# Kernel optimization log

Measured on AMD Instinct MI355X. Metric: run time of the kernel, lower is better.

## Reference

```python
import jax, jax.numpy as jnp
import numpy as np

B, T, C, H, K = 4, 2048, 1024, 16, 64
CHUNK = 64
NUM_LAYERS, LAYER_ID = 12, 6
D_MIX, D_DECAY = 32, 64


def setup_inputs() -> dict:
    key = jax.random.key(0)
    ks = jax.random.split(key, 12)
    x = jax.random.normal(ks[0], (B, T, C), jnp.float32)
    shift_state_in = jax.random.normal(ks[1], (B, C), jnp.float32)
    wkv_state_in = jnp.zeros((B, H, K, K), jnp.float32)

    r01 = LAYER_ID / max(NUM_LAYERS - 1, 1)
    r10 = 1.0 - LAYER_ID / NUM_LAYERS
    ddd = (np.arange(C, dtype=np.float64) / C)
    maa = lambda p: jnp.asarray((1.0 - ddd ** p).reshape(1, 1, C), jnp.float32)
    time_maa_x = maa(r10)
    time_maa_w = maa(r10)
    time_maa_k = maa(r10)
    time_maa_v = jnp.asarray((1.0 - (ddd ** r10 + 0.3 * r01)).reshape(1, 1, C), jnp.float32)
    time_maa_r = maa(0.5 * r10)
    time_maa_g = maa(0.5 * r10)
    time_maa_w1 = jax.random.uniform(ks[2], (C, D_MIX * 5), jnp.float32, -0.01, 0.01)
    time_maa_w2 = jax.random.uniform(ks[3], (5, D_MIX, C), jnp.float32, -0.01, 0.01)

    n = np.arange(C, dtype=np.float64)
    time_decay = jnp.asarray((-6 + 5 * (n / (C - 1)) ** (0.7 + 1.3 * r01)).reshape(1, 1, C), jnp.float32)
    time_decay_w1 = jax.random.uniform(ks[4], (C, D_DECAY), jnp.float32, -0.01, 0.01)
    time_decay_w2 = jax.random.uniform(ks[5], (D_DECAY, C), jnp.float32, -0.01, 0.01)

    zig = ((n + 1) % 3 - 1) * 0.1
    time_faaaa = jnp.asarray((r01 * (1 - n / (C - 1)) + zig).reshape(H, K), jnp.float32)
    lucid_temperature = jnp.ones((1, H, 1, 1), jnp.float32)

    s = 0.02
    W_r = jax.random.normal(ks[6], (C, C), jnp.float32) * s
    W_k = jax.random.normal(ks[7], (C, C), jnp.float32) * s
    W_v = jax.random.normal(ks[8], (C, C), jnp.float32) * s
    W_g = jax.random.normal(ks[9], (C, C), jnp.float32) * s
    W_o = jax.random.normal(ks[10], (C, C), jnp.float32) * s
    ln_gamma = jnp.ones((C,), jnp.float32)
    ln_beta = jnp.zeros((C,), jnp.float32)

    return dict(x=x, shift_state_in=shift_state_in, wkv_state_in=wkv_state_in,
                time_maa_x=time_maa_x, time_maa_w=time_maa_w, time_maa_k=time_maa_k,
                time_maa_v=time_maa_v, time_maa_r=time_maa_r, time_maa_g=time_maa_g,
                time_maa_w1=time_maa_w1, time_maa_w2=time_maa_w2,
                time_decay=time_decay, time_decay_w1=time_decay_w1, time_decay_w2=time_decay_w2,
                time_faaaa=time_faaaa, lucid_temperature=lucid_temperature,
                W_r=W_r, W_k=W_k, W_v=W_v, W_g=W_g, W_o=W_o,
                ln_gamma=ln_gamma, ln_beta=ln_beta)


def _forward(x, shift_state_in, wkv_state_in, time_maa_x, time_maa_w, time_maa_k,
             time_maa_v, time_maa_r, time_maa_g, time_maa_w1, time_maa_w2,
             time_decay, time_decay_w1, time_decay_w2, time_faaaa, lucid_temperature,
             W_r, W_k, W_v, W_g, W_o, ln_gamma, ln_beta):
    # ddlerp token shift
    dxprev = jnp.concatenate([shift_state_in[:, None, :], x[:, :-1]], axis=1) - x
    xxx = jnp.tanh((x + dxprev * time_maa_x) @ time_maa_w1).reshape(B, T, 5, D_MIX)
    m = jnp.einsum('btfd,fdc->fbtc', xxx, time_maa_w2)  # (5,B,T,C)
    mw, mk, mv, mr, mg = m[0], m[1], m[2], m[3], m[4]
    xw = x + dxprev * (time_maa_w + mw)
    xk = x + dxprev * (time_maa_k + mk)
    xv = x + dxprev * (time_maa_v + mv)
    xr = x + dxprev * (time_maa_r + mr)
    xg = x + dxprev * (time_maa_g + mg)

    r = xr @ W_r.T
    k = xk @ W_k.T
    v = xv @ W_v.T
    g = jax.nn.silu(xg @ W_g.T)
    w = time_decay + jnp.tanh(xw @ time_decay_w1) @ time_decay_w2

    tohead = lambda a: a.reshape(B, T, H, K).transpose(0, 2, 1, 3)  # (B,H,T,K)
    r_h, k_h, v_h = tohead(r), tohead(k), tohead(v)
    w_h = -jnp.exp(tohead(w))  # log-decay, negative
    u = time_faaaa.reshape(1, H, 1, K)
    temp = jax.nn.softplus(lucid_temperature)  # (1,H,1,1)

    n_chunks = T // CHUNK
    tochunks = lambda a: a.reshape(B, H, n_chunks, CHUNK, K).transpose(2, 0, 1, 3, 4)
    eye = jnp.eye(CHUNK, dtype=jnp.float32)
    mid = CHUNK // 2

    def step(state, inp):
        r_c, k_c, v_c, w_log = inp  # each (B,H,cs,K)
        w_cum = jnp.cumsum(w_log, axis=-2)
        w_shift = jnp.pad(w_cum[..., :-1, :], ((0, 0), (0, 0), (1, 0), (0, 0)))
        offset = w_shift[..., mid:mid + 1, :]
        r_decay = jnp.exp(jnp.clip(w_shift - offset, -30, 30))
        k_inv_decay = jnp.exp(jnp.clip(offset - w_cum, -30, 30))
        A = jnp.einsum('bhtk,bhsk->bhts', r_c * r_decay, k_c * k_inv_decay)
        A = jnp.tril(A, -1) + eye * jnp.sum(r_c * (u * k_c), axis=-1)[..., None]
        k_norm = k_c / jnp.maximum(jnp.linalg.norm(k_c, axis=-1, keepdims=True), 1e-12)
        K_gram = jnp.einsum('bhtk,bhsk->bhts', k_norm, k_norm)
        P = eye + jnp.exp(jnp.clip(temp * K_gram, -20, 20))
        P_v = jnp.linalg.solve(P, v_c)
        w_intra = jnp.exp(jnp.clip(w_cum - w_log, -30, 30))
        y = A @ P_v + (r_c * w_intra) @ state
        w_sum = jnp.sum(w_log, axis=-2, keepdims=True)  # (B,H,1,K)
        w_inter = jnp.exp(jnp.clip(w_sum - w_cum, -30, 30))
        new_state = state * jnp.exp(w_sum) + jnp.einsum('bhtk,bhtv->bhkv', k_c * w_inter, v_c)
        return new_state, y

    state_out, ys = jax.lax.scan(
        step, wkv_state_in,
        (tochunks(r_h), tochunks(k_h), tochunks(v_h), tochunks(w_h)))
    # (n,B,H,cs,K) -> (B,T,C)
    y = ys.transpose(1, 2, 0, 3, 4).reshape(B, H, T, K).transpose(0, 2, 1, 3).reshape(B, T, C)

    # GroupNorm with n_head groups, eps = 1e-5 * head_size_divisor**2
    eps = 1e-5 * 64.0
    yg = y.reshape(B, T, H, K)
    mu = yg.mean(axis=-1, keepdims=True)
    var = yg.var(axis=-1, keepdims=True)
    yn = (yg - mu) / jnp.sqrt(var + eps)
    yn = yn * ln_gamma.reshape(1, 1, H, K) + ln_beta.reshape(1, 1, H, K)
    yn = yn.reshape(B, T, C)

    out = (yn * g) @ W_o.T
    return out, x[:, -1], state_out


def reference(x, shift_state_in, wkv_state_in, time_maa_x, time_maa_w, time_maa_k,
              time_maa_v, time_maa_r, time_maa_g, time_maa_w1, time_maa_w2,
              time_decay, time_decay_w1, time_decay_w2, time_faaaa, lucid_temperature,
              W_r, W_k, W_v, W_g, W_o, ln_gamma, ln_beta):
    return _forward(x, shift_state_in, wkv_state_in, time_maa_x, time_maa_w, time_maa_k,
                    time_maa_v, time_maa_r, time_maa_g, time_maa_w1, time_maa_w2,
                    time_decay, time_decay_w1, time_decay_w2, time_faaaa, lucid_temperature,
                    W_r, W_k, W_v, W_g, W_o, ln_gamma, ln_beta)
```

## Files before the change

kernel.cpp:

```cpp
#include <hip/hip_runtime.h>
#include <cstdint>
#include <cstddef>

typedef unsigned short ushort_t;
#define DEVI __device__ __forceinline__

constexpr int Bc = 4, Tc = 2048, Cc = 1024, Hc = 16;
constexpr int BT = Bc * Tc;
constexpr int NCHUNK = Tc / 64;

using f32x4  = __attribute__((ext_vector_type(4))) float;
using bf16x8 = __attribute__((ext_vector_type(8))) __bf16;

DEVI ushort_t f2bf(float f) {
  union { float f; unsigned u; } v; v.f = f;
  unsigned r = v.u + 0x7fffu + ((v.u >> 16) & 1u);
  return (ushort_t)(r >> 16);
}
DEVI float bf2f(ushort_t u) {
  union { unsigned u; float f; } v; v.u = ((unsigned)u) << 16; return v.f;
}
DEVI float clip30(float x) { return fminf(fmaxf(x, -30.f), 30.f); }
DEVI float clip20(float x) { return fminf(fmaxf(x, -20.f), 20.f); }

DEVI float4 bf4up(uint2 r) {
  float4 v;
  v.x = bf2f((ushort_t)(r.x & 0xffff)); v.y = bf2f((ushort_t)(r.x >> 16));
  v.z = bf2f((ushort_t)(r.y & 0xffff)); v.w = bf2f((ushort_t)(r.y >> 16));
  return v;
}
DEVI uint2 f4pk(float4 v) {
  uint2 r;
  r.x = (unsigned)f2bf(v.x) | ((unsigned)f2bf(v.y) << 16);
  r.y = (unsigned)f2bf(v.z) | ((unsigned)f2bf(v.w) << 16);
  return r;
}

DEVI void gload_lds16(const ushort_t* g, ushort_t* l) {
  __builtin_amdgcn_global_load_lds(
      (const __attribute__((address_space(1))) void*)g,
      (__attribute__((address_space(3))) void*)l, 16, 0, 0);
}

#define GETEL(V4, E) ((E) == 0 ? (V4).x : (E) == 1 ? (V4).y : (E) == 2 ? (V4).z : (V4).w)
#define SETEL(V4, E, VAL) do { if ((E) == 0) (V4).x = (VAL); else if ((E) == 1) (V4).y = (VAL); \
                               else if ((E) == 2) (V4).z = (VAL); else (V4).w = (VAL); } while (0)

__global__ void k_xlast(const float* __restrict__ x, float* __restrict__ out) {
  int i = blockIdx.x * 256 + threadIdx.x;
  if (i >= Bc * Cc) return;
  int b = i >> 10, c = i & 1023;
  out[i] = x[((size_t)b * Tc + Tc - 1) * Cc + c];
}

__global__ void k_f2bf5(const float* __restrict__ i0, const float* __restrict__ i1,
                        const float* __restrict__ i2, const float* __restrict__ i3,
                        const float* __restrict__ i4,
                        ushort_t* __restrict__ o0, ushort_t* __restrict__ o1,
                        ushort_t* __restrict__ o2, ushort_t* __restrict__ o3,
                        ushort_t* __restrict__ o4) {
  int z = blockIdx.z;
  const float* in = (z == 0) ? i0 : (z == 1) ? i1 : (z == 2) ? i2 : (z == 3) ? i3 : i4;
  ushort_t* out   = (z == 0) ? o0 : (z == 1) ? o1 : (z == 2) ? o2 : (z == 3) ? o3 : o4;
  int i = blockIdx.x * 256 + threadIdx.x;
  if (i < Cc * Cc) out[i] = f2bf(in[i]);
}

__global__ void k_w2t(const float* __restrict__ w2, ushort_t* __restrict__ w2t) {
  int i = blockIdx.x * 256 + threadIdx.x;
  if (i >= 160 * 1024) return;
  int c = i / 160, fd = i % 160;
  w2t[i] = f2bf(w2[(size_t)fd * 1024 + c]);
}

__global__ void k_transp(const float* __restrict__ in, ushort_t* __restrict__ out, int N) {
  int i = blockIdx.x * 256 + threadIdx.x;
  if (i >= N * 1024) return;
  int n = i >> 10, r = i & 1023;
  out[i] = f2bf(in[(size_t)r * N + n]);
}

__global__ __launch_bounds__(256) void k_shift_tanh(
    const float* __restrict__ x, const float* __restrict__ sst,
    const float* __restrict__ tmx, const ushort_t* __restrict__ Wt,
    ushort_t* __restrict__ outv) {
  constexpr int NCOLS = 160, NF = NCOLS / 16;
  int tid = threadIdx.x;
  int wave = tid >> 6, lane = tid & 63;
  int row0 = (blockIdx.x * 4 + wave) * 16;
  int lr = lane & 15, lk = (lane >> 4) * 8;
  int rg = row0 + lr;
  int tt = rg & (Tc - 1);
  const float* xrow = x + (size_t)rg * Cc;
  const float* prow = (tt == 0) ? (sst + (size_t)(rg >> 11) * Cc) : (xrow - Cc);
  f32x4 acc[NF];
  #pragma unroll
  for (int n = 0; n < NF; ++n) acc[n] = (f32x4){0.f, 0.f, 0.f, 0.f};
  for (int k0 = 0; k0 < 1024; k0 += 32) {
    int c0 = k0 + lk;
    float4 xa = *(const float4*)(xrow + c0), xb = *(const float4*)(xrow + c0 + 4);
    float4 pa = *(const float4*)(prow + c0), pb = *(const float4*)(prow + c0 + 4);
    float4 ta = *(const float4*)(tmx + c0), tb = *(const float4*)(tmx + c0 + 4);
    union { bf16x8 v; uint2 u[2]; } cv;
    cv.u[0] = f4pk(make_float4(xa.x + (pa.x - xa.x) * ta.x, xa.y + (pa.y - xa.y) * ta.y,
                               xa.z + (pa.z - xa.z) * ta.z, xa.w + (pa.w - xa.w) * ta.w));
    cv.u[1] = f4pk(make_float4(xb.x + (pb.x - xb.x) * tb.x, xb.y + (pb.y - xb.y) * tb.y,
                               xb.z + (pb.z - xb.z) * tb.z, xb.w + (pb.w - xb.w) * tb.w));
    #pragma unroll
    for (int n = 0; n < NF; ++n) {
      bf16x8 b = *(const bf16x8*)&Wt[(size_t)(n * 16 + lr) * 1024 + k0 + lk];
      acc[n] = __builtin_amdgcn_mfma_f32_16x16x32_bf16(cv.v, b, acc[n], 0, 0, 0);
    }
  }
  #pragma unroll
  for (int n = 0; n < NF; ++n) {
    #pragma unroll
    for (int q = 0; q < 4; ++q) {
      int row = row0 + (lane >> 4) * 4 + q;
      size_t oi = (size_t)row * NCOLS + n * 16 + lr;
      outv[oi] = f2bf(tanhf(acc[n][q]));
    }
  }
}

template<int NCOLS, int OBF>
__global__ __launch_bounds__(256) void k_tanh_mfma(const ushort_t* __restrict__ A,
                                                   const ushort_t* __restrict__ Wt,
                                                   void* __restrict__ outv) {
  constexpr int NF = NCOLS / 16;
  int tid = threadIdx.x;
  int wave = tid >> 6, lane = tid & 63;
  int row0 = (blockIdx.x * 4 + wave) * 16;
  int lr = lane & 15, lk = (lane >> 4) * 8;
  f32x4 acc[NF];
  #pragma unroll
  for (int n = 0; n < NF; ++n) acc[n] = (f32x4){0.f, 0.f, 0.f, 0.f};
  for (int k0 = 0; k0 < 1024; k0 += 32) {
    bf16x8 a = *(const bf16x8*)&A[(size_t)(row0 + lr) * 1024 + k0 + lk];
    #pragma unroll
    for (int n = 0; n < NF; ++n) {
      bf16x8 b = *(const bf16x8*)&Wt[(size_t)(n * 16 + lr) * 1024 + k0 + lk];
      acc[n] = __builtin_amdgcn_mfma_f32_16x16x32_bf16(a, b, acc[n], 0, 0, 0);
    }
  }
  #pragma unroll
  for (int n = 0; n < NF; ++n) {
    #pragma unroll
    for (int q = 0; q < 4; ++q) {
      int row = row0 + (lane >> 4) * 4 + q;
      size_t oi = (size_t)row * NCOLS + n * 16 + lr;
      float v = tanhf(acc[n][q]);
      if (OBF == 1) ((ushort_t*)outv)[oi] = f2bf(v);
      else          ((float*)outv)[oi] = v;
    }
  }
}

__global__ __launch_bounds__(256) void k_mix5m(
    const float* __restrict__ x, const float* __restrict__ sst,
    const ushort_t* __restrict__ t160b, const ushort_t* __restrict__ w2t,
    const float* __restrict__ maaw, const float* __restrict__ maak,
    const float* __restrict__ maav, const float* __restrict__ maar,
    const float* __restrict__ maag,
    ushort_t* __restrict__ xw, ushort_t* __restrict__ xk, ushort_t* __restrict__ xv,
    ushort_t* __restrict__ xr, ushort_t* __restrict__ xg) {
  __shared__ __align__(16) ushort_t As[64 * 168];
  __shared__ __align__(16) ushort_t Bs[64 * 168];
  int tid = threadIdx.x;
  int lane = tid & 63;
  int bRow = blockIdx.x * 64, bCol = blockIdx.y * 64;
  #pragma unroll
  for (int i = 0; i < 5; ++i) {
    int e = tid + i * 256;
    int r = e / 20, cc = (e % 20) * 8;
    *(int4*)&As[r * 168 + cc] = *(const int4*)&t160b[(size_t)(bRow + r) * 160 + cc];
    *(int4*)&Bs[r * 168 + cc] = *(const int4*)&w2t[(size_t)(bCol + r) * 160 + cc];
  }
  __syncthreads();
  int wm = tid >> 7, wn = (tid >> 6) & 1;
  f32x4 acc[5][2][2];
  #pragma unroll
  for (int f = 0; f < 5; ++f)
    #pragma unroll
    for (int m = 0; m < 2; ++m)
      #pragma unroll
      for (int n = 0; n < 2; ++n) acc[f][m][n] = (f32x4){0.f, 0.f, 0.f, 0.f};
  #pragma unroll
  for (int f = 0; f < 5; ++f) {
    bf16x8 af[2], bfv[2];
    #pragma unroll
    for (int m = 0; m < 2; ++m)
      af[m] = *(const bf16x8*)&As[(wm * 32 + m * 16 + (lane & 15)) * 168 + f * 32 + (lane >> 4) * 8];
    #pragma unroll
    for (int n = 0; n < 2; ++n)
      bfv[n] = *(const bf16x8*)&Bs[(wn * 32 + n * 16 + (lane & 15)) * 168 + f * 32 + (lane >> 4) * 8];
    #pragma unroll
    for (int m = 0; m < 2; ++m)
      #pragma unroll
      for (int n = 0; n < 2; ++n)
        acc[f][m][n] = __builtin_amdgcn_mfma_f32_16x16x32_bf16(af[m], bfv[n], acc[f][m][n], 0, 0, 0);
  }
  #pragma unroll
  for (int n = 0; n < 2; ++n) {
    int col = bCol + wn * 32 + n * 16 + (lane & 15);
    float mw_c = maaw[col], mk_c = maak[col], mv_c = maav[col];
    float mr_c = maar[col], mg_c = maag[col];
    #pragma unroll
    for (int m = 0; m < 2; ++m) {
      int row0 = bRow + wm * 32 + m * 16 + (lane >> 4) * 4;
      #pragma unroll
      for (int q = 0; q < 4; ++q) {
        int rg = row0 + q;
        int tt = rg & (Tc - 1);
        size_t g = (size_t)rg * Cc + col;
        float xv0 = x[g];
        float xprev = (tt == 0) ? sst[(size_t)(rg >> 11) * Cc + col] : x[g - Cc];
        float dv = xprev - xv0;
        xw[g] = f2bf(xv0 + dv * (mw_c + acc[0][m][n][q]));
        xk[g] = f2bf(xv0 + dv * (mk_c + acc[1][m][n][q]));
        xv[g] = f2bf(xv0 + dv * (mv_c + acc[2][m][n][q]));
        xr[g] = f2bf(xv0 + dv * (mr_c + acc[3][m][n][q]));
        xg[g] = f2bf(xv0 + dv * (mg_c + acc[4][m][n][q]));
      }
    }
  }
}

template<int EPI, int OBF>
DEVI void gemm_body(const ushort_t* __restrict__ A, const ushort_t* __restrict__ Wt,
                    void* __restrict__ outv, ushort_t* As, ushort_t* Bs,
                    int bRow, int bCol) {
  int tid = threadIdx.x;
  int wave = tid >> 6, lane = tid & 63;
  int wm = wave >> 1, wn = wave & 1;
  int lr = lane >> 2;
  int lkb = (((lane & 3) ^ ((lane >> 3) & 3))) * 8;
  int pch = ((lane >> 4) ^ ((lane >> 1) & 3)) * 8;
  f32x4 zero4 = {0.f, 0.f, 0.f, 0.f};
  f32x4 acc[4][4];
  #pragma unroll
  for (int m = 0; m < 4; ++m)
    #pragma unroll
    for (int n = 0; n < 4; ++n) acc[m][n] = zero4;

  for (int k0 = 0; k0 < 1024; k0 += 32) {
    #pragma unroll
    for (int i = 0; i < 2; ++i) {
      int row = (wave + 4 * i) * 16 + lr;
      gload_lds16(A + (size_t)(bRow + row) * 1024 + k0 + lkb, &As[(wave + 4 * i) * 512]);
      gload_lds16(Wt + (size_t)(bCol + row) * 1024 + k0 + lkb, &Bs[(wave + 4 * i) * 512]);
    }
    __syncthreads();
    bf16x8 af[4], bfv[4];
    #pragma unroll
    for (int m = 0; m < 4; ++m)
      af[m] = *(const bf16x8*)&As[(wm * 64 + m * 16 + (lane & 15)) * 32 + pch];
    #pragma unroll
    for (int n = 0; n < 4; ++n)
      bfv[n] = *(const bf16x8*)&Bs[(wn * 64 + n * 16 + (lane & 15)) * 32 + pch];
    #pragma unroll
    for (int m = 0; m < 4; ++m)
      #pragma unroll
      for (int n = 0; n < 4; ++n)
        acc[m][n] = __builtin_amdgcn_mfma_f32_16x16x32_bf16(af[m], bfv[n], acc[m][n], 0, 0, 0);
    __syncthreads();
  }
  #pragma unroll
  for (int m = 0; m < 4; ++m) {
    int row = bRow + wm * 64 + m * 16 + (lane >> 4) * 4;
    #pragma unroll
    for (int n = 0; n < 4; ++n) {
      int col = bCol + wn * 64 + n * 16 + (lane & 15);
      #pragma unroll
      for (int q = 0; q < 4; ++q) {
        float v = acc[m][n][q];
        if (EPI == 1) v = v / (1.f + __expf(-v));
        size_t oi = (size_t)(row + q) * 1024 + col;
        if (OBF == 1) ((ushort_t*)outv)[oi] = f2bf(v);
        else          ((float*)outv)[oi] = v;
      }
    }
  }
}

template<int EPI, int OBF>
__global__ __launch_bounds__(256) void k_gemm_bf16(const ushort_t* __restrict__ A,
                                                   const ushort_t* __restrict__ Wt,
                                                   void* __restrict__ outv) {
  __shared__ __align__(16) ushort_t As[128 * 32];
  __shared__ __align__(16) ushort_t Bs[128 * 32];
  gemm_body<EPI, OBF>(A, Wt, outv, As, Bs, blockIdx.x * 128, blockIdx.y * 128);
}

__global__ __launch_bounds__(256) void k_gemm4(
    const ushort_t* __restrict__ A0, const ushort_t* __restrict__ A1,
    const ushort_t* __restrict__ A2, const ushort_t* __restrict__ A3,
    const ushort_t* __restrict__ W0, const ushort_t* __restrict__ W1,
    const ushort_t* __restrict__ W2, const ushort_t* __restrict__ W3,
    ushort_t* __restrict__ O0, ushort_t* __restrict__ O1,
    ushort_t* __restrict__ O2, ushort_t* __restrict__ O3) {
  __shared__ __align__(16) ushort_t As[128 * 32];
  __shared__ __align__(16) ushort_t Bs[128 * 32];
  int z = blockIdx.z;
  const ushort_t* A  = (z == 0) ? A0 : (z == 1) ? A1 : (z == 2) ? A2 : A3;
  const ushort_t* Wt = (z == 0) ? W0 : (z == 1) ? W1 : (z == 2) ? W2 : W3;
  ushort_t* out      = (z == 0) ? O0 : (z == 1) ? O1 : (z == 2) ? O2 : O3;
  if (z == 3) gemm_body<1, 1>(A, Wt, out, As, Bs, blockIdx.x * 128, blockIdx.y * 128);
  else        gemm_body<0, 1>(A, Wt, out, As, Bs, blockIdx.x * 128, blockIdx.y * 128);
}

__global__ __launch_bounds__(256) void k_preA(
    const ushort_t* __restrict__ rbuf, const ushort_t* __restrict__ kbuf,
    const ushort_t* __restrict__ vbf,
    const ushort_t* __restrict__ t64bf, const float* __restrict__ dw2,
    const float* __restrict__ tdec, const float* __restrict__ faaaa,
    ushort_t* __restrict__ rwbf, ushort_t* __restrict__ kvbf, ushort_t* __restrict__ knbuf,
    ushort_t* __restrict__ Abf, float* __restrict__ esum) {
  __shared__ __align__(16) char ubuf[16640 + 9216 + 9216];
  float* wc = (float*)ubuf;
  ushort_t* sA = (ushort_t*)(ubuf + 16640);
  ushort_t* sB = (ushort_t*)(ubuf + 16640 + 9216);
  __shared__ float sred[4 * 64];
  __shared__ float sdiag[64];
  __shared__ float snrm[64];
  int bx = blockIdx.x;
  int ci = bx & 31, bh = bx >> 5;
  int b = bh >> 4, h = bh & 15;
  int tid = threadIdx.x;
  int w = tid >> 6, lane = tid & 63;
  int c = lane;
  int row0g = b * Tc + ci * 64;
  size_t base = (size_t)row0g * Cc + (size_t)h * 64;

  #pragma unroll
  for (int j = 0; j < 2; ++j) {
    int e = tid + j * 256; int r = e >> 3, cc = (e & 7) * 8;
    *(int4*)&sA[r * 72 + cc] = *(const int4*)&t64bf[(size_t)(row0g + r) * 64 + cc];
  }
  for (int i = 0; i < 16; ++i) {
    int e = tid + i * 256; int r = e >> 6, cc = e & 63;
    sB[cc * 72 + r] = f2bf(dw2[(size_t)r * Cc + h * 64 + cc]);
  }
  float rv[16], kv[16];
  #pragma unroll
  for (int i = 0; i < 16; ++i) {
    size_t g = base + (size_t)(w * 16 + i) * Cc + c;
    rv[i] = bf2f(rbuf[g]); kv[i] = bf2f(kbuf[g]);
  }
  __syncthreads();
  {
    int rbase = w * 16;
    bf16x8 a0 = *(const bf16x8*)&sA[(rbase + (lane & 15)) * 72 + (lane >> 4) * 8];
    bf16x8 a1 = *(const bf16x8*)&sA[(rbase + (lane & 15)) * 72 + 32 + (lane >> 4) * 8];
    #pragma unroll
    for (int ct = 0; ct < 4; ++ct) {
      bf16x8 b0 = *(const bf16x8*)&sB[(ct * 16 + (lane & 15)) * 72 + (lane >> 4) * 8];
      bf16x8 b1 = *(const bf16x8*)&sB[(ct * 16 + (lane & 15)) * 72 + 32 + (lane >> 4) * 8];
      f32x4 acc = {0.f, 0.f, 0.f, 0.f};
      acc = __builtin_amdgcn_mfma_f32_16x16x32_bf16(a0, b0, acc, 0, 0, 0);
      acc = __builtin_amdgcn_mfma_f32_16x16x32_bf16(a1, b1, acc, 0, 0, 0);
      int s = ct * 16 + (lane & 15);
      #pragma unroll
      for (int q = 0; q < 4; ++q) {
        int t = rbase + (lane >> 4) * 4 + q;
        wc[t * 65 + s] = acc[q];
      }
    }
  }
  __syncthreads();
  float wv[16];
  {
    float td = tdec[h * 64 + c];
    #pragma unroll
    for (int i = 0; i < 16; ++i)
      wv[i] = -__expf(td + wc[(w * 16 + i) * 65 + c]);
  }
  {
    float s = 0.f;
    #pragma unroll
    for (int i = 0; i < 16; ++i) s += wv[i];
    sred[w * 64 + c] = s;
  }
  __syncthreads();
  {
    float run = 0.f;
    for (int ww = 0; ww < w; ++ww) run += sred[ww * 64 + c];
    #pragma unroll
    for (int i = 0; i < 16; ++i) {
      run += wv[i]; wv[i] = run;
      wc[(w * 16 + i) * 65 + c] = run;
    }
    if (w == 3) esum[((size_t)bh * 32 + ci) * 64 + c] = __expf(run);
  }
  {
    float u_c = faaaa[h * 64 + c];
    #pragma unroll
    for (int i = 0; i < 16; ++i) {
      float p = rv[i] * kv[i] * u_c;
      float n2 = kv[i] * kv[i];
      #pragma unroll
      for (int o = 32; o; o >>= 1) { p += __shfl_xor(p, o, 64); n2 += __shfl_xor(n2, o, 64); }
      if (lane == 0) {
        sdiag[w * 16 + i] = p;
        snrm[w * 16 + i] = 1.f / fmaxf(sqrtf(n2), 1e-12f);
      }
    }
  }
  __syncthreads();
  float off32 = wc[31 * 65 + c];
  float wc63 = wc[63 * 65 + c];
  #pragma unroll
  for (int i = 0; i < 16; ++i) {
    int t = w * 16 + i;
    size_t g = base + (size_t)t * Cc + c;
    float wsh = (i == 0) ? ((w == 0) ? 0.f : wc[(t - 1) * 65 + c]) : wv[i - 1];
    rwbf[g] = f2bf(rv[i] * __expf(clip30(wsh)));
    sA[t * 72 + c] = f2bf(rv[i] * __expf(clip30(wsh - off32)));
    sB[t * 72 + c] = f2bf(kv[i] * __expf(clip30(off32 - wv[i])));
    knbuf[g] = f2bf(kv[i] * snrm[t]);
  }
  __syncthreads();
  {
    int rbase = w * 16;
    bf16x8 a0 = *(const bf16x8*)&sA[(rbase + (lane & 15)) * 72 + (lane >> 4) * 8];
    bf16x8 a1 = *(const bf16x8*)&sA[(rbase + (lane & 15)) * 72 + 32 + (lane >> 4) * 8];
    #pragma unroll
    for (int ct = 0; ct < 4; ++ct) {
      bf16x8 b0 = *(const bf16x8*)&sB[(ct * 16 + (lane & 15)) * 72 + (lane >> 4) * 8];
      bf16x8 b1 = *(const bf16x8*)&sB[(ct * 16 + (lane & 15)) * 72 + 32 + (lane >> 4) * 8];
      f32x4 acc = {0.f, 0.f, 0.f, 0.f};
      acc = __builtin_amdgcn_mfma_f32_16x16x32_bf16(a0, b0, acc, 0, 0, 0);
      acc = __builtin_amdgcn_mfma_f32_16x16x32_bf16(a1, b1, acc, 0, 0, 0);
      int s = ct * 16 + (lane & 15);
      #pragma unroll
      for (int q = 0; q < 4; ++q) {
        int t = rbase + (lane >> 4) * 4 + q;
        float val = (t > s) ? acc[q] : ((t == s) ? sdiag[t] : 0.f);
        Abf[(size_t)bx * 4096 + t * 64 + s] = f2bf(val);
      }
    }
  }
  __syncthreads();
  #pragma unroll
  for (int i = 0; i < 16; ++i) {
    int t = w * 16 + i;
    size_t g = base + (size_t)t * Cc + c;
    sA[c * 72 + t] = f2bf(kv[i] * __expf(clip30(wc63 - wv[i])));
    sB[c * 72 + t] = vbf[g];
  }
  __syncthreads();
  {
    int rbase = w * 16;
    bf16x8 a0 = *(const bf16x8*)&sA[(rbase + (lane & 15)) * 72 + (lane >> 4) * 8];
    bf16x8 a1 = *(const bf16x8*)&sA[(rbase + (lane & 15)) * 72 + 32 + (lane >> 4) * 8];
    #pragma unroll
    for (int ct = 0; ct < 4; ++ct) {
      bf16x8 b0 = *(const bf16x8*)&sB[(ct * 16 + (lane & 15)) * 72 + (lane >> 4) * 8];
      bf16x8 b1 = *(const bf16x8*)&sB[(ct * 16 + (lane & 15)) * 72 + 32 + (lane >> 4) * 8];
      f32x4 acc = {0.f, 0.f, 0.f, 0.f};
      acc = __builtin_amdgcn_mfma_f32_16x16x32_bf16(a0, b0, acc, 0, 0, 0);
      acc = __builtin_amdgcn_mfma_f32_16x16x32_bf16(a1, b1, acc, 0, 0, 0);
      int j = ct * 16 + (lane & 15);
      #pragma unroll
      for (int q = 0; q < 4; ++q) {
        int ii = rbase + (lane >> 4) * 4 + q;
        kvbf[base + (size_t)ii * Cc + j] = f2bf(acc[q]);
      }
    }
  }
}

__global__ __launch_bounds__(256) void k_preB(
    const ushort_t* __restrict__ knbuf, const ushort_t* __restrict__ vbf,
    const ushort_t* __restrict__ Abf, const ushort_t* __restrict__ rwbf,
    const ushort_t* __restrict__ statebuf, const float* __restrict__ ltemp,
    const ushort_t* __restrict__ gbuf, const float* __restrict__ gamma,
    const float* __restrict__ beta, ushort_t* __restrict__ ong) {
  __shared__ __align__(16) ushort_t sKX[64 * 72];
  __shared__ __align__(16) ushort_t sAb[64 * 72];
  __shared__ __align__(16) char ubuf[64 * 72 * 2 * 2];
  __shared__ __align__(16) float pivbuf[2][192];
  __shared__ float colbuf[2][64];
  __shared__ float diagbuf[64];
  float* sP = (float*)ubuf;
  ushort_t* sRW = (ushort_t*)ubuf;
  ushort_t* sSTt = (ushort_t*)(ubuf + 64 * 72 * 2);

  int bx = blockIdx.x;
  int ci = bx & 31, bh = bx >> 5;
  int b = bh >> 4, h = bh & 15;
  int tid = threadIdx.x;
  int w = tid >> 6, lane = tid & 63;
  int rg = tid >> 4, cg = tid & 15;
  size_t base = ((size_t)(b * Tc + ci * 64)) * Cc + (size_t)h * 64;

  #pragma unroll
  for (int j = 0; j < 2; ++j) {
    int e = tid + j * 256;
    int r = e >> 3, cc = (e & 7) * 8;
    *(int4*)&sKX[r * 72 + cc] = *(const int4*)&knbuf[base + (size_t)r * Cc + cc];
    *(int4*)&sAb[r * 72 + cc] = *(const int4*)&Abf[(size_t)bx * 4096 + (size_t)r * 64 + cc];
  }
  float4 A0, A1, A2, A3, B0, B1, B2, B3;
  if (cg >= 8) {
#define LDV(R, AR, BR) do { \
      int4 raw = *(const int4*)(vbf + base + (size_t)(4 * rg + (R)) * Cc + (cg - 8) * 8); \
      (AR).x = bf2f((ushort_t)(raw.x & 0xffff)); (AR).y = bf2f((ushort_t)((unsigned)raw.x >> 16)); \
      (AR).z = bf2f((ushort_t)(raw.y & 0xffff)); (AR).w = bf2f((ushort_t)((unsigned)raw.y >> 16)); \
      (BR).x = bf2f((ushort_t)(raw.z & 0xffff)); (BR).y = bf2f((ushort_t)((unsigned)raw.z >> 16)); \
      (BR).z = bf2f((ushort_t)(raw.w & 0xffff)); (BR).w = bf2f((ushort_t)((unsigned)raw.w >> 16)); \
    } while (0)
    LDV(0, A0, B0); LDV(1, A1, B1); LDV(2, A2, B2); LDV(3, A3, B3);
#undef LDV
  }
  __syncthreads();
  float temp = log1pf(__expf(ltemp[h]));
  {
    int rbase = w * 16;
    bf16x8 a0 = *(const bf16x8*)&sKX[(rbase + (lane & 15)) * 72 + (lane >> 4) * 8];
    bf16x8 a1 = *(const bf16x8*)&sKX[(rbase + (lane & 15)) * 72 + 32 + (lane >> 4) * 8];
    #pragma unroll
    for (int ct = 0; ct < 4; ++ct) {
      bf16x8 b0 = *(const bf16x8*)&sKX[(ct * 16 + (lane & 15)) * 72 + (lane >> 4) * 8];
      bf16x8 b1 = *(const bf16x8*)&sKX[(ct * 16 + (lane & 15)) * 72 + 32 + (lane >> 4) * 8];
      f32x4 acc = {0.f, 0.f, 0.f, 0.f};
      acc = __builtin_amdgcn_mfma_f32_16x16x32_bf16(a0, b0, acc, 0, 0, 0);
      acc = __builtin_amdgcn_mfma_f32_16x16x32_bf16(a1, b1, acc, 0, 0, 0);
      int s = ct * 16 + (lane & 15);
      #pragma unroll
      for (int q = 0; q < 4; ++q) {
        int t = rbase + (lane >> 4) * 4 + q;
        sP[t * 68 + s] = ((t == s) ? 1.f : 0.f) + __expf(clip20(temp * acc[q]));
      }
    }
  }
  __syncthreads();
  if (cg < 8) {
    A0 = *(float4*)&sP[(4 * rg + 0) * 68 + cg * 8]; B0 = *(float4*)&sP[(4 * rg + 0) * 68 + cg * 8 + 4];
    A1 = *(float4*)&sP[(4 * rg + 1) * 68 + cg * 8]; B1 = *(float4*)&sP[(4 * rg + 1) * 68 + cg * 8 + 4];
    A2 = *(float4*)&sP[(4 * rg + 2) * 68 + cg * 8]; B2 = *(float4*)&sP[(4 * rg + 2) * 68 + cg * 8 + 4];
    A3 = *(float4*)&sP[(4 * rg + 3) * 68 + cg * 8]; B3 = *(float4*)&sP[(4 * rg + 3) * 68 + cg * 8 + 4];
  }
  __syncthreads();
  #pragma unroll
  for (int j = 0; j < 2; ++j) {
    int e = tid + j * 256;
    int r = e >> 3, cc = (e & 7) * 8;
    *(int4*)&sRW[r * 72 + cc] = *(const int4*)&rwbf[base + (size_t)r * Cc + cc];
  }
  {
    const ushort_t* sb = statebuf + ((size_t)bh * 32 + ci) * 4096;
    #pragma unroll
    for (int i = 0; i < 16; ++i) {
      int e = tid + i * 256;
      int r = e >> 6, c = e & 63;
      sSTt[c * 72 + r] = sb[e];
    }
  }
#define UPD(MA, MB, F) do { \
    (MA).x -= (F) * p0_.x; (MA).y -= (F) * p0_.y; (MA).z -= (F) * p0_.z; (MA).w -= (F) * p0_.w; \
    (MB).x -= (F) * p1_.x; (MB).y -= (F) * p1_.y; (MB).z -= (F) * p1_.z; (MB).w -= (F) * p1_.w; \
  } while (0)
#define GJSTEP(JL, PRA, PRB, H0, H1, H2, H3) do { \
    int j_ = jh * 8 + (JL); \
    if (rg == (j_ >> 2)) { \
      *(float4*)&pivbuf[(JL) & 1][cg * 12]     = (PRA); \
      *(float4*)&pivbuf[(JL) & 1][cg * 12 + 4] = (PRB); \
    } \
    if (cg == jh) { \
      float4 cv_; \
      cv_.x = GETEL(H0, (JL) & 3); \
      cv_.y = GETEL(H1, (JL) & 3); \
      cv_.z = GETEL(H2, (JL) & 3); \
      cv_.w = GETEL(H3, (JL) & 3); \
      *(float4*)&colbuf[(JL) & 1][rg * 4] = cv_; \
    } \
    __syncthreads(); \
    float pd_ = pivbuf[(JL) & 1][(j_ >> 3) * 12 + (j_ & 7)]; \
    float4 fv_ = *(float4*)&colbuf[(JL) & 1][rg * 4]; \
    float4 p0_ = *(float4*)&pivbuf[(JL) & 1][cg * 12]; \
    float4 p1_ = *(float4*)&pivbuf[(JL) & 1][cg * 12 + 4]; \
    if (rg == (j_ >> 2)) SETEL(fv_, (JL) & 3, 0.f); \
    float inv_ = 1.f / pd_; \
    float f0_ = fv_.x * inv_, f1_ = fv_.y * inv_, f2_ = fv_.z * inv_, f3_ = fv_.w * inv_; \
    UPD(A0, B0, f0_); UPD(A1, B1, f1_); UPD(A2, B2, f2_); UPD(A3, B3, f3_); \
  } while (0)
  for (int jh = 0; jh < 8; ++jh) {
    GJSTEP(0, A0, B0, A0, A1, A2, A3);
    GJSTEP(1, A1, B1, A0, A1, A2, A3);
    GJSTEP(2, A2, B2, A0, A1, A2, A3);
    GJSTEP(3, A3, B3, A0, A1, A2, A3);
    GJSTEP(4, A0, B0, B0, B1, B2, B3);
    GJSTEP(5, A1, B1, B0, B1, B2, B3);
    GJSTEP(6, A2, B2, B0, B1, B2, B3);
    GJSTEP(7, A3, B3, B0, B1, B2, B3);
  }
#undef GJSTEP
#undef UPD
  if (cg == (rg >> 1)) {
    float4 h0 = (rg & 1) ? B0 : A0;
    float4 h1 = (rg & 1) ? B1 : A1;
    float4 h2 = (rg & 1) ? B2 : A2;
    float4 h3 = (rg & 1) ? B3 : A3;
    *(float4*)&diagbuf[rg * 4] = make_float4(h0.x, h1.y, h2.z, h3.w);
  }
  __syncthreads();
  if (cg >= 8) {
    float4 dg = *(float4*)&diagbuf[rg * 4];
#define WRX(R, AR, BR, IR) do { \
      int cb_ = (cg - 8) * 8; \
      sKX[(cb_ + 0) * 72 + 4 * rg + (R)] = f2bf((AR).x * (IR)); \
      sKX[(cb_ + 1) * 72 + 4 * rg + (R)] = f2bf((AR).y * (IR)); \
      sKX[(cb_ + 2) * 72 + 4 * rg + (R)] = f2bf((AR).z * (IR)); \
      sKX[(cb_ + 3) * 72 + 4 * rg + (R)] = f2bf((AR).w * (IR)); \
      sKX[(cb_ + 4) * 72 + 4 * rg + (R)] = f2bf((BR).x * (IR)); \
      sKX[(cb_ + 5) * 72 + 4 * rg + (R)] = f2bf((BR).y * (IR)); \
      sKX[(cb_ + 6) * 72 + 4 * rg + (R)] = f2bf((BR).z * (IR)); \
      sKX[(cb_ + 7) * 72 + 4 * rg + (R)] = f2bf((BR).w * (IR)); \
    } while (0)
    WRX(0, A0, B0, 1.f / dg.x);
    WRX(1, A1, B1, 1.f / dg.y);
    WRX(2, A2, B2, 1.f / dg.z);
    WRX(3, A3, B3, 1.f / dg.w);
#undef WRX
  }
  __syncthreads();
  {
    int rbase = w * 16;
    bf16x8 aA0 = *(const bf16x8*)&sAb[(rbase + (lane & 15)) * 72 + (lane >> 4) * 8];
    bf16x8 aA1 = *(const bf16x8*)&sAb[(rbase + (lane & 15)) * 72 + 32 + (lane >> 4) * 8];
    bf16x8 aR0 = *(const bf16x8*)&sRW[(rbase + (lane & 15)) * 72 + (lane >> 4) * 8];
    bf16x8 aR1 = *(const bf16x8*)&sRW[(rbase + (lane & 15)) * 72 + 32 + (lane >> 4) * 8];
    f32x4 yv[4];
    #pragma unroll
    for (int ct = 0; ct < 4; ++ct) {
      bf16x8 bX0 = *(const bf16x8*)&sKX[(ct * 16 + (lane & 15)) * 72 + (lane >> 4) * 8];
      bf16x8 bX1 = *(const bf16x8*)&sKX[(ct * 16 + (lane & 15)) * 72 + 32 + (lane >> 4) * 8];
      bf16x8 bS0 = *(const bf16x8*)&sSTt[(ct * 16 + (lane & 15)) * 72 + (lane >> 4) * 8];
      bf16x8 bS1 = *(const bf16x8*)&sSTt[(ct * 16 + (lane & 15)) * 72 + 32 + (lane >> 4) * 8];
      f32x4 acc = {0.f, 0.f, 0.f, 0.f};
      acc = __builtin_amdgcn_mfma_f32_16x16x32_bf16(aA0, bX0, acc, 0, 0, 0);
      acc = __builtin_amdgcn_mfma_f32_16x16x32_bf16(aA1, bX1, acc, 0, 0, 0);
      acc = __builtin_amdgcn_mfma_f32_16x16x32_bf16(aR0, bS0, acc, 0, 0, 0);
      acc = __builtin_amdgcn_mfma_f32_16x16x32_bf16(aR1, bS1, acc, 0, 0, 0);
      yv[ct] = acc;
    }
    #pragma unroll
    for (int q = 0; q < 4; ++q) {
      float s1 = yv[0][q] + yv[1][q] + yv[2][q] + yv[3][q];
      float s2 = yv[0][q] * yv[0][q] + yv[1][q] * yv[1][q] +
                 yv[2][q] * yv[2][q] + yv[3][q] * yv[3][q];
      #pragma unroll
      for (int o = 1; o < 16; o <<= 1) {
        s1 += __shfl_xor(s1, o, 64);
        s2 += __shfl_xor(s2, o, 64);
      }
      float mu = s1 * (1.f / 64.f);
      float var = s2 * (1.f / 64.f) - mu * mu;
      float rs = rsqrtf(var + 6.4e-4f);
      int t = rbase + (lane >> 4) * 4 + q;
      #pragma unroll
      for (int ct = 0; ct < 4; ++ct) {
        int cc = ct * 16 + (lane & 15);
        size_t g = base + (size_t)t * Cc + cc;
        float yn = (yv[ct][q] - mu) * rs;
        float o = (yn * gamma[h * 64 + cc] + beta[h * 64 + cc]) * bf2f(gbuf[g]);
        ong[g] = f2bf(o);
      }
    }
  }
}

__global__ __launch_bounds__(128) void k_scanstate(
    const float* __restrict__ wkv0, const ushort_t* __restrict__ kvbf,
    const float* __restrict__ esum, ushort_t* __restrict__ statebuf,
    float* __restrict__ stout) {
  int bh = blockIdx.x >> 3;
  int rg = blockIdx.x & 7;
  int b = bh >> 4, h = bh & 15;
  int tid = threadIdx.x;
  int r = rg * 8 + (tid >> 4);
  int c0 = (tid & 15) * 4;
  float4 st = *(const float4*)(wkv0 + ((size_t)bh * 64 + r) * 64 + c0);
  size_t kvb = (size_t)(b * Tc) * Cc + (size_t)h * 64 + (size_t)r * Cc + c0;
  uint2 kvn = *(const uint2*)(kvbf + kvb);
  float4 evn = *(const float4*)(esum + (size_t)bh * 32 * 64 + c0);
  for (int ci = 0; ci < NCHUNK; ++ci) {
    *(uint2*)(statebuf + ((size_t)bh * 32 + ci) * 4096 + (size_t)r * 64 + c0) = f4pk(st);
    float4 kv = bf4up(kvn);
    float4 ev = evn;
    if (ci < NCHUNK - 1) {
      kvn = *(const uint2*)(kvbf + kvb + (size_t)(ci + 1) * 64 * Cc);
      evn = *(const float4*)(esum + ((size_t)bh * 32 + ci + 1) * 64 + c0);
    }
    st.x = st.x * ev.x + kv.x;
    st.y = st.y * ev.y + kv.y;
    st.z = st.z * ev.z + kv.z;
    st.w = st.w * ev.w + kv.w;
  }
  *(float4*)(stout + ((size_t)bh * 64 + r) * 64 + c0) = st;
}

extern "C" void kernel_launch(void* const* d_in, const int* in_sizes, int n_in,
                              void* d_out, int out_size, void* d_ws, size_t ws_size,
                              hipStream_t stream) {
  (void)in_sizes; (void)n_in; (void)out_size;
  const float* x     = (const float*)d_in[0];
  const float* sst   = (const float*)d_in[1];
  const float* wkv0  = (const float*)d_in[2];
  const float* tmx   = (const float*)d_in[3];
  const float* tmw   = (const float*)d_in[4];
  const float* tmk   = (const float*)d_in[5];
  const float* tmv   = (const float*)d_in[6];
  const float* tmr   = (const float*)d_in[7];
  const float* tmg   = (const float*)d_in[8];
  const float* w1    = (const float*)d_in[9];
  const float* w2    = (const float*)d_in[10];
  const float* tdec  = (const float*)d_in[11];
  const float* dw1   = (const float*)d_in[12];
  const float* dw2   = (const float*)d_in[13];
  const float* faaaa = (const float*)d_in[14];
  const float* ltemp = (const float*)d_in[15];
  const float* Wr    = (const float*)d_in[16];
  const float* Wk    = (const float*)d_in[17];
  const float* Wv    = (const float*)d_in[18];
  const float* Wg    = (const float*)d_in[19];
  const float* Wo    = (const float*)d_in[20];
  const float* lng   = (const float*)d_in[21];
  const float* lnb   = (const float*)d_in[22];
  float* out = (float*)d_out;

  const size_t MB = 1ull << 20;
  const size_t NEED = 242 * MB;
  if (ws_size < NEED) return;

  char* p = (char*)d_ws;
  ushort_t* kbb  = (ushort_t*)(p + 0 * MB);
  ushort_t* xwb  = (ushort_t*)(p + 16 * MB);
  ushort_t* rbb  = (ushort_t*)(p + 16 * MB);
  ushort_t* kvbf = (ushort_t*)(p + 32 * MB);
  ushort_t* statebuf = (ushort_t*)(p + 96 * MB);
  ushort_t* vbuf = (ushort_t*)(p + 128 * MB);
  ushort_t* gbuf = (ushort_t*)(p + 144 * MB);
  ushort_t* xkb  = (ushort_t*)(p + 160 * MB);
  ushort_t* Abf  = (ushort_t*)(p + 160 * MB);
  ushort_t* xvb  = (ushort_t*)(p + 176 * MB);
  ushort_t* rwbf = (ushort_t*)(p + 176 * MB);
  ushort_t* xrb  = (ushort_t*)(p + 192 * MB);
  ushort_t* xgb  = (ushort_t*)(p + 208 * MB);
  ushort_t* t160b = (ushort_t*)(p + 224 * MB);
  float*    esum = (float*)(p + 224 * MB);
  ushort_t* w2t  = (ushort_t*)(p + 227 * MB);
  ushort_t* w1t  = (ushort_t*)(p + 228 * MB);
  ushort_t* dw1t = (ushort_t*)(p + 229 * MB);
  ushort_t* t64bf = (ushort_t*)(p + 230 * MB);
  ushort_t* Wrb  = (ushort_t*)(p + 232 * MB);
  ushort_t* Wkb  = (ushort_t*)(p + 234 * MB);
  ushort_t* Wvb  = (ushort_t*)(p + 236 * MB);
  ushort_t* Wgb  = (ushort_t*)(p + 238 * MB);
  ushort_t* Wob  = (ushort_t*)(p + 240 * MB);

  const int thr = 256;
  k_f2bf5<<<dim3((Cc * Cc + 255) / 256, 1, 5), thr, 0, stream>>>(
      Wr, Wk, Wv, Wg, Wo, Wrb, Wkb, Wvb, Wgb, Wob);
  k_w2t<<<(160 * 1024 + 255) / 256, thr, 0, stream>>>(w2, w2t);
  k_transp<<<(160 * 1024 + 255) / 256, thr, 0, stream>>>(w1, w1t, 160);
  k_transp<<<(64 * 1024 + 255) / 256, thr, 0, stream>>>(dw1, dw1t, 64);

  k_xlast<<<(Bc * Cc + 255) / 256, thr, 0, stream>>>(x, out + (size_t)BT * Cc);

  k_shift_tanh<<<BT / 64, thr, 0, stream>>>(x, sst, tmx, w1t, t160b);
  k_mix5m<<<dim3(BT / 64, Cc / 64), thr, 0, stream>>>(x, sst, t160b, w2t,
                                                      tmw, tmk, tmv, tmr, tmg,
                                                      xwb, xkb, xvb, xrb, xgb);
  k_tanh_mfma<64, 1><<<BT / 64, thr, 0, stream>>>(xwb, dw1t, t64bf);

  k_gemm4<<<dim3(BT / 128, Cc / 128, 4), thr, 0, stream>>>(
      xrb, xkb, xvb, xgb, Wrb, Wkb, Wvb, Wgb, rbb, kbb, vbuf, gbuf);

  k_preA<<<2048, thr, 0, stream>>>(rbb, kbb, vbuf, t64bf, dw2, tdec, faaaa,
                                   rwbf, kvbf, xgb , Abf, esum);
  k_scanstate<<<512, 128, 0, stream>>>(wkv0, kvbf, esum, statebuf,
                                       out + (size_t)BT * Cc + (size_t)Bc * Cc);
  k_preB<<<2048, thr, 0, stream>>>(xgb , vbuf, Abf, rwbf, statebuf, ltemp,
                                   gbuf, lng, lnb, xgb );

  k_gemm_bf16<0,0><<<dim3(BT / 128, Cc / 128), thr, 0, stream>>>(xgb, Wob, out);
}
```

Baseline: 403.2 us.

## Replace fused RKVG GEMM with 256x256-tile double-buffered pipelined MFMA kernel

Replaces the 128x128-tile GEMM used for the four r/k/v/g projections with a new 256x256-tile kernel using 512 threads, double-buffered LDS (As/Bs ping-pong), direct global-to-LDS loads, a swizzled LDS layout, and explicit interleaving of loads with MFMA quarters via sched_barrier, setprio and manual waitcnt. The aim is more data reuse per tile and overlap of global loads with matrix math, so the GEMM is less bound by memory and LDS traffic. The cost is 128 KB of LDS per block and a grid of only 512 blocks, which limits occupancy. The hand-written barriers and waitcnt counts also raise the risk of subtle pipeline hazards.

```diff
diff --git a/kernel.cpp b/kernel.cpp
--- a/kernel.cpp
+++ b/kernel.cpp
@@ -292,21 +292,164 @@
   gemm_body<EPI, OBF>(A, Wt, outv, As, Bs, blockIdx.x * 128, blockIdx.y * 128);
 }
 
-__global__ __launch_bounds__(256) void k_gemm4(
+template<int EPI>
+DEVI void gemm256_body(const ushort_t* __restrict__ A, const ushort_t* __restrict__ Wt,
+                       ushort_t* __restrict__ out,
+                       ushort_t* As0, ushort_t* As1, ushort_t* Bs0, ushort_t* Bs1) {
+  int tid = threadIdx.x;
+  int wid = tid >> 6, lane = tid & 63;
+  int wm = wid >> 2, wn = wid & 3;
+  int lr = lane & 15;
+  int bRow = blockIdx.x * 256, bCol = blockIdx.y * 256;
+
+  int pch  = ((lane >> 4) ^ ((lr >> 2) & 3)) * 8;
+  int off0 = lr * 32 + pch;
+  int off1 = off0 + 512;
+  int schunk = ((lane & 3) ^ ((lane >> 4) & 3)) * 8;
+  const ushort_t* Ag = A  + (size_t)(bRow + (lane >> 2)) * 1024 + schunk;
+  const ushort_t* Bg = Wt + (size_t)(bCol + (lane >> 2)) * 1024 + schunk;
+
+  f32x4 acc[8][4];
+  #pragma unroll
+  for (int m = 0; m < 8; ++m)
+    #pragma unroll
+    for (int n = 0; n < 4; ++n) acc[m][n] = (f32x4){0.f, 0.f, 0.f, 0.f};
+  bf16x8 a[4][2], b[2][2][2];
+
+#define STG(LB, GP, tile, h) do { \
+    _Pragma("unroll") \
+    for (int j = 0; j < 2; ++j) { \
+      int s = j * 8 + wid; \
+      gload_lds16((GP) + (size_t)((h) * 128 + (s >> 1) * 16) * 1024 + (tile) * 64 + (s & 1) * 32, \
+                  (LB) + ((h) * 16 + s) * 512); \
+    } } while (0)
+#define LDAF(LB, mh) do { \
+    _Pragma("unroll") \
+    for (int m = 0; m < 4; ++m) { \
+      int rg = (wm * 8 + (mh) * 4 + m) * 1024; \
+      a[m][0] = *(const bf16x8*)((LB) + rg + off0); \
+      a[m][1] = *(const bf16x8*)((LB) + rg + off1); \
+    } } while (0)
+#define LDBF(LB, nh) do { \
+    _Pragma("unroll") \
+    for (int n = 0; n < 2; ++n) { \
+      int rg = (wn * 4 + (nh) * 2 + n) * 1024; \
+      b[nh][n][0] = *(const bf16x8*)((LB) + rg + off0); \
+      b[nh][n][1] = *(const bf16x8*)((LB) + rg + off1); \
+    } } while (0)
+#define MQ(mh, nh) do { \
+    _Pragma("unroll") \
+    for (int kk = 0; kk < 2; ++kk) \
+      _Pragma("unroll") \
+      for (int m = 0; m < 4; ++m) \
+        _Pragma("unroll") \
+        for (int n = 0; n < 2; ++n) \
+          acc[(mh) * 4 + m][(nh) * 2 + n] = __builtin_amdgcn_mfma_f32_16x16x32_bf16( \
+              a[m][kk], b[nh][n][kk], acc[(mh) * 4 + m][(nh) * 2 + n], 0, 0, 0); \
+  } while (0)
+#define SB0() __builtin_amdgcn_sched_barrier(0)
+#define MID(mh, nh) do { \
+    __builtin_amdgcn_s_barrier(); \
+    asm volatile("s_waitcnt lgkmcnt(0)" ::: "memory"); \
+    SB0(); \
+    __builtin_amdgcn_s_setprio(1); \
+    MQ(mh, nh); \
+    SB0(); \
+    __builtin_amdgcn_s_setprio(0); \
+  } while (0)
+#define ENDP() do { __builtin_amdgcn_s_barrier(); SB0(); } while (0)
+#define VMW(N) asm volatile("s_waitcnt vmcnt(" #N ")" ::: "memory")
+
+  STG(As0, Ag, 0, 0); STG(As0, Ag, 0, 1);
+  STG(Bs0, Bg, 0, 0); STG(Bs0, Bg, 0, 1);
+  STG(Bs1, Bg, 1, 0); STG(Bs1, Bg, 1, 1);
+  VMW(4);
+  __builtin_amdgcn_s_barrier();
+  SB0();
+
+  #pragma unroll 1
+  for (int it = 0; it < 7; ++it) {
+    int t1 = it * 2 + 1, t2 = it * 2 + 2, t3 = it * 2 + 3;
+    LDAF(As0, 0); LDBF(Bs0, 0); SB0();
+    STG(As1, Ag, t1, 0);
+    MID(0, 0); ENDP();
+    LDBF(Bs0, 1); SB0();
+    STG(As1, Ag, t1, 1);
+    MID(0, 1); ENDP();
+    LDAF(As0, 1); SB0();
+    STG(Bs0, Bg, t2, 0);
+    MID(1, 0); ENDP();
+    STG(Bs0, Bg, t2, 1);
+    MID(1, 1); VMW(4); ENDP();
+    LDAF(As1, 0); LDBF(Bs1, 0); SB0();
+    STG(As0, Ag, t2, 0);
+    MID(0, 0); ENDP();
+    LDBF(Bs1, 1); SB0();
+    STG(As0, Ag, t2, 1);
+    MID(0, 1); ENDP();
+    LDAF(As1, 1); SB0();
+    STG(Bs1, Bg, t3, 0);
+    MID(1, 0); ENDP();
+    STG(Bs1, Bg, t3, 1);
+    MID(1, 1); VMW(4); ENDP();
+  }
+  LDAF(As0, 0); LDBF(Bs0, 0); SB0();
+  STG(As1, Ag, 15, 0);
+  MID(0, 0); ENDP();
+  LDBF(Bs0, 1); SB0();
+  STG(As1, Ag, 15, 1);
+  MID(0, 1); ENDP();
+  LDAF(As0, 1); SB0();
+  MID(1, 0); ENDP();
+  MID(1, 1); VMW(0); ENDP();
+  LDAF(As1, 0); LDBF(Bs1, 0); SB0();
+  MID(0, 0); ENDP();
+  LDBF(Bs1, 1); SB0();
+  MID(0, 1); ENDP();
+  LDAF(As1, 1); SB0();
+  MID(1, 0); ENDP();
+  MID(1, 1);
+
+#undef STG
+#undef LDAF
+#undef LDBF
+#undef MQ
+#undef SB0
+#undef MID
+#undef ENDP
+#undef VMW
+
+  #pragma unroll
+  for (int m = 0; m < 8; ++m) {
+    int row = bRow + wm * 128 + m * 16 + (lane >> 4) * 4;
+    #pragma unroll
+    for (int n = 0; n < 4; ++n) {
+      int col = bCol + wn * 64 + n * 16 + lr;
+      #pragma unroll
+      for (int q = 0; q < 4; ++q) {
+        float v = acc[m][n][q];
+        if (EPI == 1) v = v / (1.f + __expf(-v));
+        out[(size_t)(row + q) * 1024 + col] = f2bf(v);
+      }
+    }
+  }
+}
+
+__global__ __launch_bounds__(512, 2) void k_gemm4x(
     const ushort_t* __restrict__ A0, const ushort_t* __restrict__ A1,
     const ushort_t* __restrict__ A2, const ushort_t* __restrict__ A3,
     const ushort_t* __restrict__ W0, const ushort_t* __restrict__ W1,
     const ushort_t* __restrict__ W2, const ushort_t* __restrict__ W3,
     ushort_t* __restrict__ O0, ushort_t* __restrict__ O1,
     ushort_t* __restrict__ O2, ushort_t* __restrict__ O3) {
-  __shared__ __align__(16) ushort_t As[128 * 32];
-  __shared__ __align__(16) ushort_t Bs[128 * 32];
+  __shared__ __align__(16) ushort_t As[2][256 * 64];
+  __shared__ __align__(16) ushort_t Bs[2][256 * 64];
   int z = blockIdx.z;
   const ushort_t* A  = (z == 0) ? A0 : (z == 1) ? A1 : (z == 2) ? A2 : A3;
   const ushort_t* Wt = (z == 0) ? W0 : (z == 1) ? W1 : (z == 2) ? W2 : W3;
   ushort_t* out      = (z == 0) ? O0 : (z == 1) ? O1 : (z == 2) ? O2 : O3;
-  if (z == 3) gemm_body<1, 1>(A, Wt, out, As, Bs, blockIdx.x * 128, blockIdx.y * 128);
-  else        gemm_body<0, 1>(A, Wt, out, As, Bs, blockIdx.x * 128, blockIdx.y * 128);
+  if (z == 3) gemm256_body<1>(A, Wt, out, As[0], As[1], Bs[0], Bs[1]);
+  else        gemm256_body<0>(A, Wt, out, As[0], As[1], Bs[0], Bs[1]);
 }
 
 __global__ __launch_bounds__(256) void k_preA(
@@ -775,7 +918,7 @@
                                                       xwb, xkb, xvb, xrb, xgb);
   k_tanh_mfma<64, 1><<<BT / 64, thr, 0, stream>>>(xwb, dw1t, t64bf);
 
-  k_gemm4<<<dim3(BT / 128, Cc / 128, 4), thr, 0, stream>>>(
+  k_gemm4x<<<dim3(BT / 256, Cc / 256, 4), 512, 0, stream>>>(
       xrb, xkb, xvb, xgb, Wrb, Wkb, Wvb, Wgb, rbb, kbb, vbuf, gbuf);
 
   k_preA<<<2048, thr, 0, stream>>>(rbb, kbb, vbuf, t64bf, dw2, tdec, faaaa,
```

New measurement: 437.1 us. 8.4% more time.

## Double-buffer LDS tiles in bf16 GEMM to overlap global loads with MFMA

Applied to the files above, without the earlier changes.

The bf16 GEMM body now keeps two LDS stages for A and B. It issues the direct-to-LDS global loads for the next 32-wide K slice before running the MFMAs on the current one, with the loop unrolled by two to alternate buffers. The aim is to hide global-load latency behind MFMA work instead of stalling after each load. In exchange, LDS use per block doubles to 32KB, which may lower occupancy, and correctness depends on the barrier placement between buffer reuse.

```diff
diff --git a/kernel.cpp b/kernel.cpp
--- a/kernel.cpp
+++ b/kernel.cpp
@@ -243,28 +243,42 @@
     #pragma unroll
     for (int n = 0; n < 4; ++n) acc[m][n] = zero4;
 
-  for (int k0 = 0; k0 < 1024; k0 += 32) {
-    #pragma unroll
-    for (int i = 0; i < 2; ++i) {
-      int row = (wave + 4 * i) * 16 + lr;
-      gload_lds16(A + (size_t)(bRow + row) * 1024 + k0 + lkb, &As[(wave + 4 * i) * 512]);
-      gload_lds16(Wt + (size_t)(bCol + row) * 1024 + k0 + lkb, &Bs[(wave + 4 * i) * 512]);
-    }
+#define STAGEK(OFS, K0) do { \
+    _Pragma("unroll") \
+    for (int i = 0; i < 2; ++i) { \
+      int row = (wave + 4 * i) * 16 + lr; \
+      gload_lds16(A + (size_t)(bRow + row) * 1024 + (K0) + lkb, &As[(OFS) + (wave + 4 * i) * 512]); \
+      gload_lds16(Wt + (size_t)(bCol + row) * 1024 + (K0) + lkb, &Bs[(OFS) + (wave + 4 * i) * 512]); \
+    } } while (0)
+#define CMP(OFS) do { \
+    bf16x8 af[4], bfv[4]; \
+    _Pragma("unroll") \
+    for (int m = 0; m < 4; ++m) \
+      af[m] = *(const bf16x8*)&As[(OFS) + (wm * 64 + m * 16 + (lane & 15)) * 32 + pch]; \
+    _Pragma("unroll") \
+    for (int n = 0; n < 4; ++n) \
+      bfv[n] = *(const bf16x8*)&Bs[(OFS) + (wn * 64 + n * 16 + (lane & 15)) * 32 + pch]; \
+    _Pragma("unroll") \
+    for (int m = 0; m < 4; ++m) \
+      _Pragma("unroll") \
+      for (int n = 0; n < 4; ++n) \
+        acc[m][n] = __builtin_amdgcn_mfma_f32_16x16x32_bf16(af[m], bfv[n], acc[m][n], 0, 0, 0); \
+  } while (0)
+
+  STAGEK(0, 0);
+  __syncthreads();
+  #pragma unroll 1
+  for (int k0 = 0; k0 < 1024; k0 += 64) {
+    STAGEK(4096, k0 + 32);
+    CMP(0);
     __syncthreads();
-    bf16x8 af[4], bfv[4];
-    #pragma unroll
-    for (int m = 0; m < 4; ++m)
-      af[m] = *(const bf16x8*)&As[(wm * 64 + m * 16 + (lane & 15)) * 32 + pch];
-    #pragma unroll
-    for (int n = 0; n < 4; ++n)
-      bfv[n] = *(const bf16x8*)&Bs[(wn * 64 + n * 16 + (lane & 15)) * 32 + pch];
-    #pragma unroll
-    for (int m = 0; m < 4; ++m)
-      #pragma unroll
-      for (int n = 0; n < 4; ++n)
-        acc[m][n] = __builtin_amdgcn_mfma_f32_16x16x32_bf16(af[m], bfv[n], acc[m][n], 0, 0, 0);
+    if (k0 + 64 < 1024) STAGEK(0, k0 + 64);
+    CMP(4096);
     __syncthreads();
   }
+#undef STAGEK
+#undef CMP
+
   #pragma unroll
   for (int m = 0; m < 4; ++m) {
     int row = bRow + wm * 64 + m * 16 + (lane >> 4) * 4;
@@ -287,8 +301,8 @@
 __global__ __launch_bounds__(256) void k_gemm_bf16(const ushort_t* __restrict__ A,
                                                    const ushort_t* __restrict__ Wt,
                                                    void* __restrict__ outv) {
-  __shared__ __align__(16) ushort_t As[128 * 32];
-  __shared__ __align__(16) ushort_t Bs[128 * 32];
+  __shared__ __align__(16) ushort_t As[2 * 128 * 32];
+  __shared__ __align__(16) ushort_t Bs[2 * 128 * 32];
   gemm_body<EPI, OBF>(A, Wt, outv, As, Bs, blockIdx.x * 128, blockIdx.y * 128);
 }
 
@@ -299,8 +313,8 @@
     const ushort_t* __restrict__ W2, const ushort_t* __restrict__ W3,
     ushort_t* __restrict__ O0, ushort_t* __restrict__ O1,
     ushort_t* __restrict__ O2, ushort_t* __restrict__ O3) {
-  __shared__ __align__(16) ushort_t As[128 * 32];
-  __shared__ __align__(16) ushort_t Bs[128 * 32];
+  __shared__ __align__(16) ushort_t As[2 * 128 * 32];
+  __shared__ __align__(16) ushort_t Bs[2 * 128 * 32];
   int z = blockIdx.z;
   const ushort_t* A  = (z == 0) ? A0 : (z == 1) ? A1 : (z == 2) ? A2 : A3;
   const ushort_t* Wt = (z == 0) ? W0 : (z == 1) ? W1 : (z == 2) ? W2 : W3;
```

Result: slower. 434.3 us (+7.7%).
